# Kernel optimization log

Hardware: AMD Instinct MI355X
Metric: run time of the kernel (lower is better)

The kernel has to match this reference:

```python
import jax, jax.numpy as jnp
import numpy as np

D_MODEL = 1024
HEADS = 4
DK = 1024          # key_dim = d_model * expand_k
DV = 2048          # value_dim = d_model * expand_v
HDK = DK // HEADS  # 256
HDV = DV // HEADS  # 512
LOW_RANK = 16
CHUNK = 64
GATE_NORM = 16.0
EPS = 1e-5


def setup_inputs() -> dict:
    key = jax.random.key(0)
    ks = jax.random.split(key, 10)
    gain = 2.0 ** (-2.5)

    def xavier(k, shape):  # shape = (fan_in, fan_out); stored as [in, out]
        lim = gain * np.sqrt(6.0 / (shape[0] + shape[1]))
        return jax.random.uniform(k, shape, jnp.float32, -lim, lim)

    return {
        'x': jax.random.normal(ks[0], (2, 2048, D_MODEL), jnp.float32),
        'Wq': xavier(ks[1], (D_MODEL, DK)),
        'Wk': xavier(ks[2], (D_MODEL, DK)),
        'Wv': xavier(ks[3], (D_MODEL, DV)),
        'Wg': xavier(ks[4], (D_MODEL, DV)),
        'Wgk1': xavier(ks[5], (D_MODEL, LOW_RANK)),
        'Wgk2': xavier(ks[6], (LOW_RANK, DK)),
        'bgk2': jnp.zeros((DK,), jnp.float32),
        'Wo': xavier(ks[7], (DV, D_MODEL)),
        'rms_w': jnp.ones((HDV,), jnp.float32),
    }


def _gla_chunked(q, k, v, g):
    """Gated linear attention: S_t = exp(g_t) (*) S_{t-1} + k_t^T v_t;  o_t = scale * q_t @ S_t.
    q,k,g: [B,H,T,HDK]; v: [B,H,T,HDV]. Chunk-parallel formulation, scan over chunks."""
    B, H, T, _ = q.shape
    NC = T // CHUNK
    scale = HDK ** -0.5

    def to_chunks(t, d):  # [B,H,T,d] -> [NC,B,H,CHUNK,d]
        return t.reshape(B, H, NC, CHUNK, d).transpose(2, 0, 1, 3, 4)

    qc = to_chunks(q, HDK)
    kc = to_chunks(k, HDK)
    vc = to_chunks(v, HDV)
    bc = jnp.cumsum(to_chunks(g, HDK), axis=-2)  # inclusive log-decay within chunk
    mask = jnp.tril(jnp.ones((CHUNK, CHUNK), bool))

    def step(S, inp):
        qb, kb, vb, bb = inp                       # [B,H,C,HDK/HDV]
        qg = qb * jnp.exp(bb) * scale              # queries decayed to chunk start
        kd = kb * jnp.exp(-bb)                     # keys un-decayed (intra)
        A = jnp.einsum('bhtd,bhsd->bhts', qg, kd)  # intra-chunk scores
        A = jnp.where(mask, A, 0.0)
        o = jnp.einsum('bhts,bhsv->bhtv', A, vb) + jnp.einsum('bhtd,bhdv->bhtv', qg, S)
        b_last = bb[:, :, -1:, :]                  # [B,H,1,HDK]
        kg = kb * jnp.exp(b_last - bb)             # keys decayed to chunk end
        S = S * jnp.exp(b_last[:, :, 0, :])[..., None] + jnp.einsum('bhtd,bhtv->bhdv', kg, vb)
        return S, o

    S0 = jnp.zeros((B, H, HDK, HDV), q.dtype)
    _, o = jax.lax.scan(step, S0, (qc, kc, vc, bc))  # o: [NC,B,H,C,HDV]
    return o.transpose(1, 2, 0, 3, 4).reshape(B, H, T, HDV)


def reference(x, Wq, Wk, Wv, Wg, Wgk1, Wgk2, bgk2, Wo, rms_w):
    B, T, _ = x.shape
    q = (x @ Wq).reshape(B, T, HEADS, HDK).transpose(0, 2, 1, 3)
    k = (x @ Wk).reshape(B, T, HEADS, HDK).transpose(0, 2, 1, 3)
    v = (x @ Wv).reshape(B, T, HEADS, HDV).transpose(0, 2, 1, 3)
    gk = (x @ Wgk1) @ Wgk2 + bgk2                       # low-rank gate logits
    g = jax.nn.log_sigmoid(gk.astype(jnp.float32)) / GATE_NORM
    g = g.reshape(B, T, HEADS, HDK).transpose(0, 2, 1, 3)

    o = _gla_chunked(q, k, v, g)                        # [B,H,T,HDV]
    o = o.transpose(0, 2, 1, 3)                         # [B,T,H,HDV]
    o = o * jax.lax.rsqrt(jnp.mean(o * o, axis=-1, keepdims=True) + EPS) * rms_w
    o = o.reshape(B, T, HEADS * HDV)
    o = o * jax.nn.silu(x @ Wg)
    return o @ Wo
```

## Files before the change

kernel.cpp:

```cpp
#include <hip/hip_runtime.h>
#include <hip/hip_bf16.h>
#include <math.h>

#define TOK  4096
#define DM   1024
#define DKC  1024
#define DVC  2048
#define NH   4
#define HDK_ 256
#define HDV_ 512
#define NCH  32
#define CHK  64

typedef __attribute__((ext_vector_type(8))) short bf16x8;
typedef __attribute__((ext_vector_type(4))) float f32x4;

__device__ inline float bf2f(short s) {
    unsigned int b = ((unsigned int)(unsigned short)s) << 16;
    return __uint_as_float(b);
}
__device__ inline short f2bf_bits(float f) {
    __hip_bfloat16 h = __float2bfloat16(f);
    return *reinterpret_cast<short*>(&h);
}

__device__ __forceinline__ void gl_lds16(const void* g, void* l) {
    __builtin_amdgcn_global_load_lds((const __attribute__((address_space(1))) void*)g,
                                     (__attribute__((address_space(3))) void*)l, 16, 0, 0);
}

__global__ __launch_bounds__(256) void prep_x(const float* __restrict__ x,
                                              const float* __restrict__ W1,
                                              const float* __restrict__ W2,
                                              const float* __restrict__ b2,
                                              __hip_bfloat16* __restrict__ xb,
                                              float* __restrict__ g) {
    __shared__ float xl[1024];
    __shared__ float red[16][17];
    __shared__ float t1l[16];
    const int t = blockIdx.x, tid = threadIdx.x;
    float4 xv = *reinterpret_cast<const float4*>(&x[(size_t)t * DM + tid * 4]);
    *reinterpret_cast<float4*>(&xl[tid * 4]) = xv;
    short4 xs;
    xs.x = f2bf_bits(xv.x); xs.y = f2bf_bits(xv.y);
    xs.z = f2bf_bits(xv.z); xs.w = f2bf_bits(xv.w);
    *reinterpret_cast<short4*>((short*)xb + (size_t)t * DM + tid * 4) = xs;
    __syncthreads();
    const int o = tid & 15, p = tid >> 4;
    float s = 0.f;
#pragma unroll 8
    for (int m = 0; m < 64; ++m) {
        int kk = p * 64 + m;
        s += xl[kk] * W1[kk * 16 + o];
    }
    red[p][o] = s;
    __syncthreads();
    if (tid < 16) {
        float tot = 0.f;
#pragma unroll
        for (int pp = 0; pp < 16; ++pp) tot += red[pp][tid];
        t1l[tid] = tot;
    }
    __syncthreads();
#pragma unroll
    for (int j = 0; j < 4; ++j) {
        int c = tid + j * 256;
        float acc = b2[c];
#pragma unroll
        for (int r = 0; r < 16; ++r) acc += t1l[r] * W2[r * 1024 + c];
        float ls = fminf(acc, 0.f) - log1pf(expf(-fabsf(acc)));
        g[(size_t)t * DKC + c] = ls * (1.f / 16.f);
    }
}

__global__ __launch_bounds__(256) void convT(const float* __restrict__ W,
                                             __hip_bfloat16* __restrict__ Wt,
                                             int K, int N) {
    __shared__ float tile[32][33];
    int n0 = blockIdx.x * 32, k0 = blockIdx.y * 32;
    int tx = threadIdx.x & 31, ty = threadIdx.x >> 5;
#pragma unroll
    for (int i = 0; i < 32; i += 8)
        tile[ty + i][tx] = W[(size_t)(k0 + ty + i) * N + n0 + tx];
    __syncthreads();
#pragma unroll
    for (int i = 0; i < 32; i += 8)
        Wt[(size_t)(n0 + ty + i) * K + k0 + tx] = __float2bfloat16(tile[tx][ty + i]);
}

__global__ __launch_bounds__(512) void gemm256(const __hip_bfloat16* __restrict__ A,
                                               const __hip_bfloat16* __restrict__ Wt,
                                               __hip_bfloat16* __restrict__ qo,
                                               __hip_bfloat16* __restrict__ ko,
                                               __hip_bfloat16* __restrict__ vT,
                                               __hip_bfloat16* __restrict__ xgo) {
    __shared__ __align__(16) short SM[9 * 8192];
    const int K = 1024, NT = 16;
    const int tid = threadIdx.x;
    const int wave = tid >> 6, lane = tid & 63;
    const int wr = wave >> 2;
    const int wc = wave & 3;
    const int hc = wc >> 1;
    const int l15 = lane & 15, kb = lane >> 4;
    const int m0 = blockIdx.y * 128, n0 = blockIdx.x * 256;

    const bool isV = (n0 >= 2048 && n0 < 4096);
    __hip_bfloat16* dst = nullptr; int ldd = 0, nloc0 = 0;
    if (n0 < 1024)       { dst = qo;  ldd = 1024; nloc0 = n0; }
    else if (n0 < 2048)  { dst = ko;  ldd = 1024; nloc0 = n0 - 1024; }
    else if (n0 >= 4096) { dst = xgo; ldd = 2048; nloc0 = n0 - 4096; }

    f32x4 acc[4][4];
#pragma unroll
    for (int mf = 0; mf < 4; ++mf)
#pragma unroll
        for (int nf = 0; nf < 4; ++nf) acc[mf][nf] = (f32x4){0.f, 0.f, 0.f, 0.f};

    auto stage_unit = [&](int u) {
        int tk = u / 3, p = u % 3;
        int slot = u % 9;
#pragma unroll
        for (int j = 0; j < 2; ++j) {
            int row = (wave * 2 + j) * 8 + (lane >> 3);
            int srcg = (lane & 7) ^ (row & 7);
            const __hip_bfloat16* src =
                (p == 0) ? &A[(size_t)(m0 + row) * K + tk * 64 + srcg * 8]
                         : &Wt[(size_t)(n0 + (p - 1) * 128 + row) * K + tk * 64 + srcg * 8];
            gl_lds16(src, &SM[slot * 8192 + (wave * 2 + j) * 512]);
        }
    };

    for (int u = 0; u <= 5; ++u) stage_unit(u);

    for (int t = 0; t < NT; ++t) {
        if (t < NT - 1) asm volatile("s_waitcnt vmcnt(6)" ::: "memory");
        else            asm volatile("s_waitcnt vmcnt(0)" ::: "memory");
        __builtin_amdgcn_sched_barrier(0);
        __builtin_amdgcn_s_barrier();

        {
            int u1 = 3 * t + 8;
            if (u1 > 3 * NT - 1) u1 = 3 * NT - 1;
            for (int u = 3 * t + 6; u <= u1; ++u) stage_unit(u);
        }

        const short* Abase = &SM[((3 * t) % 9) * 8192];
        const short* Bbase = &SM[((3 * t + 1 + hc) % 9) * 8192];
#pragma unroll
        for (int kk = 0; kk < 2; ++kk) {
            bf16x8 a[4], bfr[4];
#pragma unroll
            for (int mf = 0; mf < 4; ++mf) {
                int row = wr * 64 + mf * 16 + l15;
                int gsw = (kk * 4 + kb) ^ (row & 7);
                a[mf] = *reinterpret_cast<const bf16x8*>(&Abase[row * 64 + gsw * 8]);
            }
#pragma unroll
            for (int nf = 0; nf < 4; ++nf) {
                int row = (wc & 1) * 64 + nf * 16 + l15;
                int gsw = (kk * 4 + kb) ^ (row & 7);
                bfr[nf] = *reinterpret_cast<const bf16x8*>(&Bbase[row * 64 + gsw * 8]);
            }
            __builtin_amdgcn_s_setprio(1);
#pragma unroll
            for (int mf = 0; mf < 4; ++mf)
#pragma unroll
                for (int nf = 0; nf < 4; ++nf)
                    acc[mf][nf] = __builtin_amdgcn_mfma_f32_16x16x32_bf16(a[mf], bfr[nf], acc[mf][nf], 0, 0, 0);
            __builtin_amdgcn_s_setprio(0);
        }
    }

    if (!isV) {
#pragma unroll
        for (int mf = 0; mf < 4; ++mf)
#pragma unroll
            for (int nf = 0; nf < 4; ++nf)
#pragma unroll
                for (int r = 0; r < 4; ++r)
                    dst[(size_t)(m0 + wr * 64 + mf * 16 + kb * 4 + r) * ldd +
                        nloc0 + wc * 64 + nf * 16 + l15] = __float2bfloat16(acc[mf][nf][r]);
    } else {
        __syncthreads();
        short* Cl = SM;
#pragma unroll
        for (int mf = 0; mf < 4; ++mf)
#pragma unroll
            for (int nf = 0; nf < 4; ++nf)
#pragma unroll
                for (int r = 0; r < 4; ++r) {
                    int trow = wr * 64 + mf * 16 + kb * 4 + r;
                    int vcol = wc * 64 + nf * 16 + l15;
                    Cl[vcol * 132 + trow] = f2bf_bits(acc[mf][nf][r]);
                }
        __syncthreads();
        const int vcg0 = n0 - 2048;
        const int bh = (m0 >> 11) * NH + (vcg0 >> 9);
        const int vl0 = vcg0 & 511;
        const int tl0 = m0 & 2047;
        short* vTs = (short*)vT;
#pragma unroll
        for (int it = 0; it < 8; ++it) {
            int idx = tid + it * 512;
            int row = idx >> 4;
            int c8 = (idx & 15) * 8;
            bf16x8 vv = *reinterpret_cast<const bf16x8*>(&Cl[row * 132 + c8]);
            *reinterpret_cast<bf16x8*>(
                &vTs[((size_t)(bh * 512 + vl0 + row)) * 2048 + tl0 + c8]) = vv;
        }
    }
}

__global__ __launch_bounds__(256) void gemm_bf16(const __hip_bfloat16* __restrict__ A,
                                                 const __hip_bfloat16* __restrict__ Wt,
                                                 float* __restrict__ C,
                                                 int M, int N, int K) {
    __shared__ __align__(16) short Buf[2][2][128 * 64];
    const int tid = threadIdx.x;
    const int wave = tid >> 6, lane = tid & 63;
    const int wr = wave >> 1, wc = wave & 1;
    const int m0 = blockIdx.y * 128, n0 = blockIdx.x * 128;
    const int l15 = lane & 15, kb = lane >> 4;
    const int lr8 = lane >> 3, lc8 = (lane & 7) * 8;
    const int NT = K >> 6;

    f32x4 acc[4][4];
#pragma unroll
    for (int mf = 0; mf < 4; ++mf)
#pragma unroll
        for (int nf = 0; nf < 4; ++nf) acc[mf][nf] = (f32x4){0.f, 0.f, 0.f, 0.f};

#define STAGE_G(kt, bi)                                                          \
    {                                                                            \
        int k0s = (kt) * 64;                                                     \
        _Pragma("unroll")                                                        \
        for (int j = 0; j < 4; ++j) {                                            \
            int inst = wave * 4 + j;                                             \
            int r = inst * 8 + lr8;                                              \
            gl_lds16(&A[(size_t)(m0 + r) * K + k0s + lc8], &Buf[bi][0][inst * 512]); \
            gl_lds16(&Wt[(size_t)(n0 + r) * K + k0s + lc8], &Buf[bi][1][inst * 512]); \
        }                                                                        \
    }

    STAGE_G(0, 0);
    STAGE_G(1, 1);

    for (int t = 0; t < NT; ++t) {
        if (t + 1 < NT) asm volatile("s_waitcnt vmcnt(8)" ::: "memory");
        else            asm volatile("s_waitcnt vmcnt(0)" ::: "memory");
        __builtin_amdgcn_sched_barrier(0);
        __builtin_amdgcn_s_barrier();
        const short* Ab = Buf[t & 1][0];
        const short* Bb = Buf[t & 1][1];
#pragma unroll
        for (int kk = 0; kk < 2; ++kk) {
            bf16x8 af[4], bfr[4];
#pragma unroll
            for (int mf = 0; mf < 4; ++mf)
                af[mf] = *reinterpret_cast<const bf16x8*>(&Ab[(wr * 64 + mf * 16 + l15) * 64 + kk * 32 + kb * 8]);
#pragma unroll
            for (int nf = 0; nf < 4; ++nf)
                bfr[nf] = *reinterpret_cast<const bf16x8*>(&Bb[(wc * 64 + nf * 16 + l15) * 64 + kk * 32 + kb * 8]);
#pragma unroll
            for (int mf = 0; mf < 4; ++mf)
#pragma unroll
                for (int nf = 0; nf < 4; ++nf)
                    acc[mf][nf] = __builtin_amdgcn_mfma_f32_16x16x32_bf16(af[mf], bfr[nf], acc[mf][nf], 0, 0, 0);
        }
        asm volatile("s_waitcnt lgkmcnt(0)" ::: "memory");
        __builtin_amdgcn_sched_barrier(0);
        __builtin_amdgcn_s_barrier();
        if (t + 2 < NT) STAGE_G(t + 2, t & 1);
    }
#undef STAGE_G

#pragma unroll
    for (int mf = 0; mf < 4; ++mf)
#pragma unroll
        for (int nf = 0; nf < 4; ++nf)
#pragma unroll
            for (int r = 0; r < 4; ++r)
                C[(size_t)(m0 + wr * 64 + mf * 16 + kb * 4 + r) * N + n0 + wc * 64 + nf * 16 + l15] =
                    acc[mf][nf][r];
}

__global__ __launch_bounds__(256) void gla_chunk(const __hip_bfloat16* __restrict__ qb,
                                                 const __hip_bfloat16* __restrict__ kb,
                                                 const __hip_bfloat16* __restrict__ vT,
                                                 const float* __restrict__ g,
                                                 __hip_bfloat16* __restrict__ qg,
                                                 __hip_bfloat16* __restrict__ kgT,
                                                 __hip_bfloat16* __restrict__ o1,
                                                 float* __restrict__ dlast) {
    __shared__ __align__(16) short SM[36864];
    short* qg_l = SM;
    short* kd_l = SM + 16384;
    short* V_l  = SM;
    short* Am_l = SM + 32768;

    const int chunk = blockIdx.x, bh = blockIdx.y;
    const int b = bh >> 2, h = bh & 3;
    const int t0 = b * 2048 + chunk * 64;
    const int tt0 = chunk * 64;
    const int tid = threadIdx.x;
    const float scale = 0.0625f;

    {
        const int d = tid;
        const float* gcol = g + (size_t)t0 * DKC + h * HDK_ + d;
        const __hip_bfloat16* qcol = qb + (size_t)t0 * DKC + h * HDK_ + d;
        const __hip_bfloat16* kcol = kb + (size_t)t0 * DKC + h * HDK_ + d;
        float run = 0.f;
#pragma unroll
        for (int i = 0; i < 64; ++i) run += gcol[(size_t)i * DKC];
        const float ebl = expf(run);
        dlast[((size_t)bh * NCH + chunk) * HDK_ + d] = ebl;

        bf16x8 kreg[8];
        run = 0.f;
#pragma unroll
        for (int i = 0; i < 64; ++i) {
            run += gcol[(size_t)i * DKC];
            float eb = expf(run);
            float qv = __bfloat162float(qcol[(size_t)i * DKC]) * eb * scale;
            float kdv = __bfloat162float(kcol[(size_t)i * DKC]) * expf(-run);
            qg[(size_t)(t0 + i) * DKC + h * HDK_ + d] = __float2bfloat16(qv);
            int bq = ((i * 512 + d * 2) ^ ((i & 7) << 4)) >> 1;
            qg_l[bq] = f2bf_bits(qv);
            kd_l[bq] = f2bf_bits(kdv);
            kreg[i >> 3][i & 7] = f2bf_bits(kdv * ebl);
        }
        __hip_bfloat16* kdst = kgT + ((size_t)(bh * HDK_ + d)) * 2048 + chunk * 64;
#pragma unroll
        for (int j = 0; j < 8; ++j)
            *reinterpret_cast<bf16x8*>(&kdst[j * 8]) = kreg[j];
    }
    __syncthreads();

    const int wv = tid >> 6, lane = tid & 63;
    const int l15 = lane & 15, kb_ = lane >> 4;

    {
        f32x4 accA[4];
#pragma unroll
        for (int sf = 0; sf < 4; ++sf) accA[sf] = (f32x4){0.f, 0.f, 0.f, 0.f};
        const int trow = wv * 16 + l15;
#pragma unroll
        for (int ks = 0; ks < 8; ++ks) {
            bf16x8 af = *reinterpret_cast<const bf16x8*>(
                &qg_l[((trow * 512 + (ks * 32 + kb_ * 8) * 2) ^ ((trow & 7) << 4)) >> 1]);
#pragma unroll
            for (int sf = 0; sf < 4; ++sf) {
                int srow = sf * 16 + l15;
                bf16x8 bfr = *reinterpret_cast<const bf16x8*>(
                    &kd_l[((srow * 512 + (ks * 32 + kb_ * 8) * 2) ^ ((srow & 7) << 4)) >> 1]);
                accA[sf] = __builtin_amdgcn_mfma_f32_16x16x32_bf16(af, bfr, accA[sf], 0, 0, 0);
            }
        }
#pragma unroll
        for (int sf = 0; sf < 4; ++sf)
#pragma unroll
            for (int r = 0; r < 4; ++r) {
                int t = wv * 16 + kb_ * 4 + r, s = sf * 16 + l15;
                float val = (t >= s) ? accA[sf][r] : 0.f;
                Am_l[((t * 128 + s * 2) ^ ((t & 7) << 4)) >> 1] = f2bf_bits(val);
            }
    }
    __syncthreads();

    {
        const int lr8 = lane >> 3, slot = lane & 7;
#pragma unroll
        for (int i8 = 0; i8 < 16; ++i8) {
            int vrow0 = wv * 128 + i8 * 8;
            const __hip_bfloat16* src =
                &vT[((size_t)bh * 512 + vrow0 + lr8) * 2048 + tt0 + (slot ^ (lr8 & 7)) * 8];
            gl_lds16(src, &V_l[vrow0 * 64]);
        }
    }
    __syncthreads();

    {
        f32x4 accO[4][8];
#pragma unroll
        for (int tf = 0; tf < 4; ++tf)
#pragma unroll
            for (int vf = 0; vf < 8; ++vf) accO[tf][vf] = (f32x4){0.f, 0.f, 0.f, 0.f};
#pragma unroll
        for (int kk = 0; kk < 2; ++kk) {
            bf16x8 af[4];
#pragma unroll
            for (int tf = 0; tf < 4; ++tf) {
                int row = tf * 16 + l15;
                af[tf] = *reinterpret_cast<const bf16x8*>(
                    &Am_l[((row * 128 + (kk * 32 + kb_ * 8) * 2) ^ ((row & 7) << 4)) >> 1]);
            }
#pragma unroll
            for (int vf = 0; vf < 8; ++vf) {
                int rv = wv * 128 + vf * 16 + l15;
                bf16x8 bfr = *reinterpret_cast<const bf16x8*>(
                    &V_l[((rv * 128 + (kk * 32 + kb_ * 8) * 2) ^ ((rv & 7) << 4)) >> 1]);
#pragma unroll
                for (int tf = 0; tf < 4; ++tf)
                    accO[tf][vf] = __builtin_amdgcn_mfma_f32_16x16x32_bf16(af[tf], bfr, accO[tf][vf], 0, 0, 0);
            }
        }
#pragma unroll
        for (int tf = 0; tf < 4; ++tf)
#pragma unroll
            for (int vf = 0; vf < 8; ++vf)
#pragma unroll
                for (int r = 0; r < 4; ++r) {
                    int t = tf * 16 + kb_ * 4 + r;
                    int vv = wv * 128 + vf * 16 + l15;
                    o1[(size_t)(t0 + t) * DVC + h * HDV_ + vv] = __float2bfloat16(accO[tf][vf][r]);
                }
    }
}

__global__ __launch_bounds__(256) void u_pass(const __hip_bfloat16* __restrict__ vT,
                                              const __hip_bfloat16* __restrict__ kgT,
                                              __hip_bfloat16* __restrict__ U) {
    __shared__ __align__(16) short Av[128 * 64];
    __shared__ __align__(16) short Bv[128 * 64];
    const int bx = blockIdx.x, c = blockIdx.y, bh = blockIdx.z;
    const int vc0 = (bx >> 1) * 128, d0 = (bx & 1) * 128;
    const int tid = threadIdx.x;
    const int wave = tid >> 6, lane = tid & 63;
    const int wr = wave >> 1, wc = wave & 1;
    const int l15 = lane & 15, kb = lane >> 4;
    const int lr8 = lane >> 3, lc8 = (lane & 7) * 8;

#pragma unroll
    for (int j = 0; j < 4; ++j) {
        int inst = wave * 4 + j;
        int r = inst * 8 + lr8;
        gl_lds16(&vT[((size_t)bh * 512 + vc0 + r) * 2048 + c * 64 + lc8], &Av[inst * 512]);
        gl_lds16(&kgT[((size_t)bh * HDK_ + d0 + r) * 2048 + c * 64 + lc8], &Bv[inst * 512]);
    }
    __syncthreads();

    f32x4 acc[4][4];
#pragma unroll
    for (int mf = 0; mf < 4; ++mf)
#pragma unroll
        for (int nf = 0; nf < 4; ++nf) acc[mf][nf] = (f32x4){0.f, 0.f, 0.f, 0.f};
#pragma unroll
    for (int kk = 0; kk < 2; ++kk) {
        bf16x8 af[4], bfr[4];
#pragma unroll
        for (int mf = 0; mf < 4; ++mf)
            af[mf] = *reinterpret_cast<const bf16x8*>(&Av[(wr * 64 + mf * 16 + l15) * 64 + kk * 32 + kb * 8]);
#pragma unroll
        for (int nf = 0; nf < 4; ++nf)
            bfr[nf] = *reinterpret_cast<const bf16x8*>(&Bv[(wc * 64 + nf * 16 + l15) * 64 + kk * 32 + kb * 8]);
#pragma unroll
        for (int mf = 0; mf < 4; ++mf)
#pragma unroll
            for (int nf = 0; nf < 4; ++nf)
                acc[mf][nf] = __builtin_amdgcn_mfma_f32_16x16x32_bf16(af[mf], bfr[nf], acc[mf][nf], 0, 0, 0);
    }
    const size_t Ub = ((size_t)bh * NCH + c) * 131072;
#pragma unroll
    for (int mf = 0; mf < 4; ++mf)
#pragma unroll
        for (int nf = 0; nf < 4; ++nf)
#pragma unroll
            for (int r = 0; r < 4; ++r) {
                int vc = vc0 + wr * 64 + mf * 16 + kb * 4 + r;
                int d = d0 + wc * 64 + nf * 16 + l15;
                U[Ub + (size_t)vc * 256 + d] = __float2bfloat16(acc[mf][nf][r]);
            }
}

__global__ __launch_bounds__(256) void scan_pass(__hip_bfloat16* __restrict__ U,
                                                 const float* __restrict__ dlast) {
    int gid = blockIdx.x * 256 + threadIdx.x;
    int bh = gid >> 14;
    int rem = gid & 16383;
    int vc = rem >> 5;
    int dg = rem & 31;
    float S[8];
#pragma unroll
    for (int j = 0; j < 8; ++j) S[j] = 0.f;
    size_t base = (size_t)bh * NCH * 131072 + (size_t)vc * 256 + dg * 8;
    for (int c = 0; c < NCH; ++c) {
        __hip_bfloat16* p = U + base + (size_t)c * 131072;
        bf16x8 u = *reinterpret_cast<bf16x8*>(p);
        const float* dl = &dlast[((size_t)bh * NCH + c) * HDK_ + dg * 8];
        float4 e0 = *reinterpret_cast<const float4*>(dl);
        float4 e1 = *reinterpret_cast<const float4*>(dl + 4);
        float e[8] = {e0.x, e0.y, e0.z, e0.w, e1.x, e1.y, e1.z, e1.w};
        bf16x8 outv;
#pragma unroll
        for (int j = 0; j < 8; ++j) {
            outv[j] = f2bf_bits(S[j]);
            S[j] = S[j] * e[j] + bf2f(u[j]);
        }
        *reinterpret_cast<bf16x8*>(p) = outv;
    }
}

__global__ __launch_bounds__(256) void o_pass(const __hip_bfloat16* __restrict__ qg,
                                              const __hip_bfloat16* __restrict__ U,
                                              const __hip_bfloat16* __restrict__ o1,
                                              __hip_bfloat16* __restrict__ o2) {
    __shared__ __align__(16) char smem[64 * 132 * 4];
    short* Av = (short*)smem;
    short* Bv = (short*)smem + 128 * 64;
    float* oT = (float*)smem;
    const int vt = blockIdx.x, c = blockIdx.y, bh = blockIdx.z;
    const int b = bh >> 2, h = bh & 3;
    const int vc0 = vt * 128;
    const int t0 = b * 2048 + c * 64;
    const int tid = threadIdx.x;
    const int wave = tid >> 6, lane = tid & 63;
    const int wr = wave >> 1, wc = wave & 1;
    const int l15 = lane & 15, kb = lane >> 4;
    const int lr8 = lane >> 3, lc8 = (lane & 7) * 8;
    const size_t Ub = ((size_t)bh * NCH + c) * 131072;

    f32x4 acc[4][2];
#pragma unroll
    for (int mf = 0; mf < 4; ++mf)
#pragma unroll
        for (int nf = 0; nf < 2; ++nf) acc[mf][nf] = (f32x4){0.f, 0.f, 0.f, 0.f};

    for (int ks = 0; ks < 4; ++ks) {
        const int d0 = ks * 64;
#pragma unroll
        for (int j = 0; j < 4; ++j) {
            int inst = wave * 4 + j;
            int r = inst * 8 + lr8;
            gl_lds16(&U[Ub + (size_t)(vc0 + r) * 256 + d0 + lc8], &Av[inst * 512]);
        }
#pragma unroll
        for (int j = 0; j < 2; ++j) {
            int inst = wave * 2 + j;
            int r = inst * 8 + lr8;
            gl_lds16(&qg[(size_t)(t0 + r) * DKC + h * HDK_ + d0 + lc8], &Bv[inst * 512]);
        }
        __syncthreads();
#pragma unroll
        for (int kk = 0; kk < 2; ++kk) {
            bf16x8 af[4], bfr[2];
#pragma unroll
            for (int mf = 0; mf < 4; ++mf)
                af[mf] = *reinterpret_cast<const bf16x8*>(&Av[(wr * 64 + mf * 16 + l15) * 64 + kk * 32 + kb * 8]);
#pragma unroll
            for (int nf = 0; nf < 2; ++nf)
                bfr[nf] = *reinterpret_cast<const bf16x8*>(&Bv[(wc * 32 + nf * 16 + l15) * 64 + kk * 32 + kb * 8]);
#pragma unroll
            for (int mf = 0; mf < 4; ++mf)
#pragma unroll
                for (int nf = 0; nf < 2; ++nf)
                    acc[mf][nf] = __builtin_amdgcn_mfma_f32_16x16x32_bf16(af[mf], bfr[nf], acc[mf][nf], 0, 0, 0);
        }
        __syncthreads();
    }
#pragma unroll
    for (int mf = 0; mf < 4; ++mf)
#pragma unroll
        for (int nf = 0; nf < 2; ++nf)
#pragma unroll
            for (int r = 0; r < 4; ++r)
                oT[(wc * 32 + nf * 16 + l15) * 132 + wr * 64 + mf * 16 + kb * 4 + r] = acc[mf][nf][r];
    __syncthreads();
#pragma unroll
    for (int j = 0; j < 4; ++j) {
        int t = (tid >> 4) + j * 16;
        int vc8 = (tid & 15) * 8;
        float4 a0 = *reinterpret_cast<const float4*>(&oT[t * 132 + vc8]);
        float4 a1 = *reinterpret_cast<const float4*>(&oT[t * 132 + vc8 + 4]);
        size_t oi = (size_t)(t0 + t) * DVC + h * HDV_ + vc0 + vc8;
        bf16x8 iv = *reinterpret_cast<const bf16x8*>(&o1[oi]);
        bf16x8 outv;
        outv[0] = f2bf_bits(a0.x + bf2f(iv[0]));
        outv[1] = f2bf_bits(a0.y + bf2f(iv[1]));
        outv[2] = f2bf_bits(a0.z + bf2f(iv[2]));
        outv[3] = f2bf_bits(a0.w + bf2f(iv[3]));
        outv[4] = f2bf_bits(a1.x + bf2f(iv[4]));
        outv[5] = f2bf_bits(a1.y + bf2f(iv[5]));
        outv[6] = f2bf_bits(a1.z + bf2f(iv[6]));
        outv[7] = f2bf_bits(a1.w + bf2f(iv[7]));
        *reinterpret_cast<bf16x8*>((__hip_bfloat16*)o2 + oi) = outv;
    }
}

__global__ __launch_bounds__(256) void rms_gate(const __hip_bfloat16* __restrict__ o2,
                                                const __hip_bfloat16* __restrict__ xg,
                                                const float* __restrict__ rms_w,
                                                __hip_bfloat16* __restrict__ gated) {
    __shared__ float wsum[4];
    const int th = blockIdx.x;
    const int t = th >> 2, h = th & 3;
    const int tid = threadIdx.x;
    const size_t base = (size_t)t * DVC + h * HDV_;
    short2 ov = reinterpret_cast<const short2*>((const short*)o2 + base)[tid];
    float v0 = bf2f(ov.x), v1 = bf2f(ov.y);
    float s = v0 * v0 + v1 * v1;
#pragma unroll
    for (int off = 32; off >= 1; off >>= 1) s += __shfl_down(s, off, 64);
    if ((tid & 63) == 0) wsum[tid >> 6] = s;
    __syncthreads();
    float tot = wsum[0] + wsum[1] + wsum[2] + wsum[3];
    float rms = rsqrtf(tot * (1.f / 512.f) + 1e-5f);
    short2 gv = reinterpret_cast<const short2*>((const short*)xg + base)[tid];
    float g0 = bf2f(gv.x), g1 = bf2f(gv.y);
    float s0 = g0 / (1.f + expf(-g0));
    float s1 = g1 / (1.f + expf(-g1));
    float2 w = reinterpret_cast<const float2*>(rms_w)[tid];
    short2 outp;
    outp.x = f2bf_bits(v0 * rms * w.x * s0);
    outp.y = f2bf_bits(v1 * rms * w.y * s1);
    reinterpret_cast<short2*>((short*)gated + base)[tid] = outp;
}

extern "C" void kernel_launch(void* const* d_in, const int* in_sizes, int n_in,
                              void* d_out, int out_size, void* d_ws, size_t ws_size,
                              hipStream_t stream) {
    const float* x    = (const float*)d_in[0];
    const float* Wq   = (const float*)d_in[1];
    const float* Wk   = (const float*)d_in[2];
    const float* Wv   = (const float*)d_in[3];
    const float* Wg   = (const float*)d_in[4];
    const float* Wgk1 = (const float*)d_in[5];
    const float* Wgk2 = (const float*)d_in[6];
    const float* bgk2 = (const float*)d_in[7];
    const float* Wo   = (const float*)d_in[8];
    const float* rmsw = (const float*)d_in[9];
    float* out = (float*)d_out;
    float* ws = (float*)d_ws;

    const size_t M1 = 1ull << 20;
    __hip_bfloat16* xb    = (__hip_bfloat16*)ws;
    __hip_bfloat16* WtAll = (__hip_bfloat16*)(ws + 2 * M1);
    __hip_bfloat16* q_b   = (__hip_bfloat16*)(ws + 5 * M1);
    __hip_bfloat16* k_b   = (__hip_bfloat16*)(ws + 7 * M1);
    float*          g     = ws + 13 * M1;
    __hip_bfloat16* U     = (__hip_bfloat16*)ws;
    __hip_bfloat16* xg_b  = (__hip_bfloat16*)(ws + 17 * M1);
    __hip_bfloat16* qgb   = (__hip_bfloat16*)(ws + 21 * M1);
    __hip_bfloat16* kgT   = (__hip_bfloat16*)(ws + 23 * M1);
    __hip_bfloat16* vT    = (__hip_bfloat16*)(ws + 25 * M1);
    __hip_bfloat16* o1    = (__hip_bfloat16*)(ws + 29 * M1);
    __hip_bfloat16* o2    = (__hip_bfloat16*)(ws + 33 * M1);
    float*          dlast = ws + 37 * M1 + 65536;
    __hip_bfloat16* WtO   = (__hip_bfloat16*)(ws + 23 * M1);
    __hip_bfloat16* gated = (__hip_bfloat16*)(ws + 25 * M1);

    prep_x<<<TOK, 256, 0, stream>>>(x, Wgk1, Wgk2, bgk2, xb, g);
    convT<<<dim3(32, 32), 256, 0, stream>>>(Wq, WtAll,                    DM, DKC);
    convT<<<dim3(32, 32), 256, 0, stream>>>(Wk, WtAll + 1024 * 1024,      DM, DKC);
    convT<<<dim3(64, 32), 256, 0, stream>>>(Wv, WtAll + 2048 * 1024,      DM, DVC);
    convT<<<dim3(64, 32), 256, 0, stream>>>(Wg, WtAll + 4096 * 1024,      DM, DVC);

    gemm256<<<dim3(24, 32), 512, 0, stream>>>(xb, WtAll, q_b, k_b, vT, xg_b);

    gla_chunk<<<dim3(NCH, 8), 256, 0, stream>>>(q_b, k_b, vT, g, qgb, kgT, o1, dlast);

    u_pass<<<dim3(8, NCH, 8), 256, 0, stream>>>(vT, kgT, U);
    scan_pass<<<512, 256, 0, stream>>>(U, dlast);
    o_pass<<<dim3(4, NCH, 8), 256, 0, stream>>>(qgb, U, o1, o2);

    convT<<<dim3(32, 64), 256, 0, stream>>>(Wo, WtO, DVC, DM);
    rms_gate<<<TOK * NH, 256, 0, stream>>>(o2, xg_b, rmsw, gated);
    gemm_bf16<<<dim3(8, 32), 256, 0, stream>>>(gated, WtO, out, TOK, DM, DVC);
}
```

Before: 250.9 us.

## Merge weight transposes into one launch and interleave staging with MFMA in gemm256

All five weight transpose/convert launches are folded into a single kernel, and the Wo transpose moves to a separate workspace slot so it can run at the start. In gemm256, the global-to-LDS staging is split across two half-steps and interleaved with the two k-substeps. Each half loads fragments, issues some staging, then runs its MFMAs behind an extra barrier. This is meant to cut launch overhead and to hide load latency behind matrix math. In exchange each main-loop iteration gains an extra barrier, and register pressure may rise.

```diff
diff --git a/kernel.cpp b/kernel.cpp
--- a/kernel.cpp
+++ b/kernel.cpp
@@ -73,12 +73,24 @@
     }
 }
 
-__global__ __launch_bounds__(256) void convT(const float* __restrict__ W,
-                                             __hip_bfloat16* __restrict__ Wt,
-                                             int K, int N) {
+__global__ __launch_bounds__(256) void convT_all(const float* __restrict__ Wq,
+                                                 const float* __restrict__ Wk,
+                                                 const float* __restrict__ Wv,
+                                                 const float* __restrict__ Wg,
+                                                 const float* __restrict__ Wo,
+                                                 __hip_bfloat16* __restrict__ WtAll,
+                                                 __hip_bfloat16* __restrict__ WtO) {
     __shared__ float tile[32][33];
-    int n0 = blockIdx.x * 32, k0 = blockIdx.y * 32;
-    int tx = threadIdx.x & 31, ty = threadIdx.x >> 5;
+    int bid = blockIdx.x;
+    const float* W; __hip_bfloat16* Wt; int K, N, r;
+    if (bid < 1024)      { W = Wq; Wt = WtAll;               K = 1024; N = 1024; r = bid; }
+    else if (bid < 2048) { W = Wk; Wt = WtAll + 1024 * 1024; K = 1024; N = 1024; r = bid - 1024; }
+    else if (bid < 4096) { W = Wv; Wt = WtAll + 2048 * 1024; K = 1024; N = 2048; r = bid - 2048; }
+    else if (bid < 6144) { W = Wg; Wt = WtAll + 4096 * 1024; K = 1024; N = 2048; r = bid - 4096; }
+    else                 { W = Wo; Wt = WtO;                 K = 2048; N = 1024; r = bid - 6144; }
+    const int ncols = N >> 5;
+    const int n0 = (r % ncols) * 32, k0 = (r / ncols) * 32;
+    const int tx = threadIdx.x & 31, ty = threadIdx.x >> 5;
 #pragma unroll
     for (int i = 0; i < 32; i += 8)
         tile[ty + i][tx] = W[(size_t)(k0 + ty + i) * N + n0 + tx];
@@ -132,43 +144,68 @@
 
     for (int u = 0; u <= 5; ++u) stage_unit(u);
 
+    const int ULAST = 3 * NT - 1;
     for (int t = 0; t < NT; ++t) {
         if (t < NT - 1) asm volatile("s_waitcnt vmcnt(6)" ::: "memory");
         else            asm volatile("s_waitcnt vmcnt(0)" ::: "memory");
         __builtin_amdgcn_sched_barrier(0);
         __builtin_amdgcn_s_barrier();
 
-        {
-            int u1 = 3 * t + 8;
-            if (u1 > 3 * NT - 1) u1 = 3 * NT - 1;
-            for (int u = 3 * t + 6; u <= u1; ++u) stage_unit(u);
-        }
-
         const short* Abase = &SM[((3 * t) % 9) * 8192];
         const short* Bbase = &SM[((3 * t + 1 + hc) % 9) * 8192];
-#pragma unroll
-        for (int kk = 0; kk < 2; ++kk) {
-            bf16x8 a[4], bfr[4];
-#pragma unroll
-            for (int mf = 0; mf < 4; ++mf) {
-                int row = wr * 64 + mf * 16 + l15;
-                int gsw = (kk * 4 + kb) ^ (row & 7);
-                a[mf] = *reinterpret_cast<const bf16x8*>(&Abase[row * 64 + gsw * 8]);
-            }
-#pragma unroll
-            for (int nf = 0; nf < 4; ++nf) {
-                int row = (wc & 1) * 64 + nf * 16 + l15;
-                int gsw = (kk * 4 + kb) ^ (row & 7);
-                bfr[nf] = *reinterpret_cast<const bf16x8*>(&Bbase[row * 64 + gsw * 8]);
-            }
-            __builtin_amdgcn_s_setprio(1);
-#pragma unroll
-            for (int mf = 0; mf < 4; ++mf)
-#pragma unroll
-                for (int nf = 0; nf < 4; ++nf)
-                    acc[mf][nf] = __builtin_amdgcn_mfma_f32_16x16x32_bf16(a[mf], bfr[nf], acc[mf][nf], 0, 0, 0);
-            __builtin_amdgcn_s_setprio(0);
-        }
+
+        bf16x8 a0[4], b0[4];
+#pragma unroll
+        for (int mf = 0; mf < 4; ++mf) {
+            int row = wr * 64 + mf * 16 + l15;
+            int gsw = (0 * 4 + kb) ^ (row & 7);
+            a0[mf] = *reinterpret_cast<const bf16x8*>(&Abase[row * 64 + gsw * 8]);
+        }
+#pragma unroll
+        for (int nf = 0; nf < 4; ++nf) {
+            int row = (wc & 1) * 64 + nf * 16 + l15;
+            int gsw = (0 * 4 + kb) ^ (row & 7);
+            b0[nf] = *reinterpret_cast<const bf16x8*>(&Bbase[row * 64 + gsw * 8]);
+        }
+        if (3 * t + 6 <= ULAST) stage_unit(3 * t + 6);
+        if (3 * t + 7 <= ULAST) stage_unit(3 * t + 7);
+        __builtin_amdgcn_sched_barrier(0);
+        __builtin_amdgcn_s_barrier();
+        asm volatile("s_waitcnt lgkmcnt(0)" ::: "memory");
+        __builtin_amdgcn_sched_barrier(0);
+        __builtin_amdgcn_s_setprio(1);
+#pragma unroll
+        for (int mf = 0; mf < 4; ++mf)
+#pragma unroll
+            for (int nf = 0; nf < 4; ++nf)
+                acc[mf][nf] = __builtin_amdgcn_mfma_f32_16x16x32_bf16(a0[mf], b0[nf], acc[mf][nf], 0, 0, 0);
+        __builtin_amdgcn_s_setprio(0);
+
+        bf16x8 a1[4], b1[4];
+#pragma unroll
+        for (int mf = 0; mf < 4; ++mf) {
+            int row = wr * 64 + mf * 16 + l15;
+            int gsw = (1 * 4 + kb) ^ (row & 7);
+            a1[mf] = *reinterpret_cast<const bf16x8*>(&Abase[row * 64 + gsw * 8]);
+        }
+#pragma unroll
+        for (int nf = 0; nf < 4; ++nf) {
+            int row = (wc & 1) * 64 + nf * 16 + l15;
+            int gsw = (1 * 4 + kb) ^ (row & 7);
+            b1[nf] = *reinterpret_cast<const bf16x8*>(&Bbase[row * 64 + gsw * 8]);
+        }
+        if (3 * t + 8 <= ULAST) stage_unit(3 * t + 8);
+        __builtin_amdgcn_sched_barrier(0);
+        __builtin_amdgcn_s_barrier();
+        asm volatile("s_waitcnt lgkmcnt(0)" ::: "memory");
+        __builtin_amdgcn_sched_barrier(0);
+        __builtin_amdgcn_s_setprio(1);
+#pragma unroll
+        for (int mf = 0; mf < 4; ++mf)
+#pragma unroll
+            for (int nf = 0; nf < 4; ++nf)
+                acc[mf][nf] = __builtin_amdgcn_mfma_f32_16x16x32_bf16(a1[mf], b1[nf], acc[mf][nf], 0, 0, 0);
+        __builtin_amdgcn_s_setprio(0);
     }
 
     if (!isV) {
@@ -646,14 +683,11 @@
     __hip_bfloat16* o1    = (__hip_bfloat16*)(ws + 29 * M1);
     __hip_bfloat16* o2    = (__hip_bfloat16*)(ws + 33 * M1);
     float*          dlast = ws + 37 * M1 + 65536;
-    __hip_bfloat16* WtO   = (__hip_bfloat16*)(ws + 23 * M1);
+    __hip_bfloat16* WtO   = (__hip_bfloat16*)(ws + 38 * M1);
     __hip_bfloat16* gated = (__hip_bfloat16*)(ws + 25 * M1);
 
+    convT_all<<<8192, 256, 0, stream>>>(Wq, Wk, Wv, Wg, Wo, WtAll, WtO);
     prep_x<<<TOK, 256, 0, stream>>>(x, Wgk1, Wgk2, bgk2, xb, g);
-    convT<<<dim3(32, 32), 256, 0, stream>>>(Wq, WtAll,                    DM, DKC);
-    convT<<<dim3(32, 32), 256, 0, stream>>>(Wk, WtAll + 1024 * 1024,      DM, DKC);
-    convT<<<dim3(64, 32), 256, 0, stream>>>(Wv, WtAll + 2048 * 1024,      DM, DVC);
-    convT<<<dim3(64, 32), 256, 0, stream>>>(Wg, WtAll + 4096 * 1024,      DM, DVC);
 
     gemm256<<<dim3(24, 32), 512, 0, stream>>>(xb, WtAll, q_b, k_b, vT, xg_b);
 
@@ -663,7 +697,6 @@
     scan_pass<<<512, 256, 0, stream>>>(U, dlast);
     o_pass<<<dim3(4, NCH, 8), 256, 0, stream>>>(qgb, U, o1, o2);
 
-    convT<<<dim3(32, 64), 256, 0, stream>>>(Wo, WtO, DVC, DM);
     rms_gate<<<TOK * NH, 256, 0, stream>>>(o2, xg_b, rmsw, gated);
     gemm_bf16<<<dim3(8, 32), 256, 0, stream>>>(gated, WtO, out, TOK, DM, DVC);
 }
```

Result: faster. 237.8 us (-5.2%).
